# Performance work log

Hardware: AMD Instinct MI355X
Metric: run time of the kernel (lower is better)

## Reference

```python
import math
import jax, jax.numpy as jnp
import numpy as np

H = 16  # head_count
D = 1024  # model_dim
DH = D // H  # dim_per_head = 64
PAD_IDX = 1


def setup_inputs() -> dict:
    key = jax.random.key(0)
    ks = jax.random.split(key, 16)
    B, L = 4, 512
    s = 0.02
    inp = {
        'key': jax.random.normal(ks[0], (B, L, D), jnp.float32),
        'value': jax.random.normal(ks[1], (B, L, D), jnp.float32),
        'query': jax.random.normal(ks[2], (B, L, D), jnp.float32),
        'ast_parents_matrix': jax.random.randint(ks[3], (B, L, L), 0, 200, jnp.int32),
        'mask': jnp.zeros((B, 1, L), jnp.bool_),
        'Wq': jax.random.normal(ks[4], (D, D), jnp.float32) * s,
        'bq': jnp.zeros((D,), jnp.float32),
        'Wk': jax.random.normal(ks[5], (D, D), jnp.float32) * s,
        'bk': jnp.zeros((D,), jnp.float32),
        'Wv': jax.random.normal(ks[6], (D, D), jnp.float32) * s,
        'bv': jnp.zeros((D,), jnp.float32),
        'Wo': jax.random.normal(ks[7], (D, D), jnp.float32) * s,
        'bo': jnp.zeros((D,), jnp.float32),
        'struct_emb': jax.random.normal(ks[8], (200, DH), jnp.float32).at[PAD_IDX].set(0.0),
        'value_emb': jax.random.normal(ks[9], (10000, DH), jnp.float32).at[PAD_IDX].set(0.0),
    }
    return inp


def _parent_embeddings(matrix, struct_emb, value_emb):
    # matrix: (B, Lq, K) int ids; even key positions use structure vocab, odd use value vocab
    B, Lq, K = matrix.shape
    s_ids = matrix[:, :, ::2]   # (B, Lq, ceil(K/2))
    v_ids = matrix[:, :, 1::2]  # (B, Lq, floor(K/2))
    emb_s = struct_emb[s_ids]   # (B, Lq, S, DH)
    emb_v = value_emb[v_ids]    # (B, Lq, V, DH)
    S = emb_s.shape[2]
    if emb_v.shape[2] != S:  # odd K: pad value stream by one zero slot, drop after interleave
        emb_v = jnp.concatenate([emb_v, jnp.zeros_like(emb_s[:, :, :1])], axis=2)
    pe = jnp.stack([emb_s, emb_v], axis=3).reshape(B, Lq, 2 * S, DH)
    return pe[:, :, :K, :]  # (B, Lq, K, DH)


def reference(key, value, query, ast_parents_matrix, mask,
              Wq, bq, Wk, bk, Wv, bv, Wo, bo, struct_emb, value_emb):
    B, L, _ = query.shape

    def shape(x):
        return x.reshape(B, -1, H, DH).transpose(0, 2, 1, 3)  # (B,H,L,DH)

    q = shape(query @ Wq + bq) / math.sqrt(DH)
    k = shape(key @ Wk + bk)
    v = shape(value @ Wv + bv)

    qk = jnp.einsum('bhid,bhjd->bhij', q, k)  # (B,H,L,L)

    pe = _parent_embeddings(ast_parents_matrix[:, :, :L], struct_emb, value_emb)
    score_ast = jnp.einsum('bhid,bijd->bhij', q, pe)

    scores = (qk + score_ast).astype(jnp.float32)
    scores = jnp.where(mask[:, None, :, :], -1e18, scores)  # mask: (B,1,L)->(B,1,1,L)
    attn = jax.nn.softmax(scores, axis=-1).astype(q.dtype)
    # dropout p=0.0 (eval) -> identity
    context = jnp.einsum('bhij,bhjd->bhid', attn, v)  # (B,H,L,DH)
    context = context.transpose(0, 2, 1, 3).reshape(B, L, D)
    output = context @ Wo + bo
    return output, attn
```

## Files before the change

### kernel.cpp

```cpp
#include <hip/hip_runtime.h>
#include <cstddef>

#define H 16
#define D 1024
#define DH 64
#define L 512

typedef __attribute__((ext_vector_type(8))) short bf16x8;
typedef __attribute__((ext_vector_type(4))) short bf16x4;
typedef __attribute__((ext_vector_type(4))) float f32x4;

__device__ inline short f2bf(float x) {
    union { float f; unsigned u; } c; c.f = x;
    unsigned r = (c.u + 0x7FFFu + ((c.u >> 16) & 1u)) >> 16;
    return (short)r;
}
__device__ inline float bf2f(short x) {
    union { float f; unsigned u; } c;
    c.u = ((unsigned)(unsigned short)x) << 16; return c.f;
}

struct CvtArgs { const float* src[5]; short* dst[5]; int n[5]; };

__global__ __launch_bounds__(256) void cvt_kernel(CvtArgs a) {
    int r = blockIdx.y;
    const float* s = a.src[r];
    short* d = a.dst[r];
    int n = a.n[r];
    int i = (blockIdx.x * 256 + threadIdx.x) * 8;
    if (i >= n) return;
    float4 x0 = *(const float4*)(s + i);
    float4 x1 = *(const float4*)(s + i + 4);
    bf16x8 o;
    o[0] = f2bf(x0.x); o[1] = f2bf(x0.y); o[2] = f2bf(x0.z); o[3] = f2bf(x0.w);
    o[4] = f2bf(x1.x); o[5] = f2bf(x1.y); o[6] = f2bf(x1.z); o[7] = f2bf(x1.w);
    *(bf16x8*)(d + i) = o;
}

struct WtArgs { const float* W[4]; short* T[4]; };

__global__ __launch_bounds__(256) void wtrans_kernel(WtArgs a) {
    const float* W = a.W[blockIdx.z];
    short* T = a.T[blockIdx.z];
    int idx = blockIdx.x * 256 + threadIdx.x;
    int n = idx & 1023;
    int k0 = (idx >> 10) << 3;
    bf16x8 o;
    #pragma unroll
    for (int kk = 0; kk < 8; ++kk)
        o[kk] = f2bf(W[(size_t)(k0 + kk) * 1024 + n]);
    *(bf16x8*)(T + (size_t)n * 1024 + k0) = o;
}

#define BM 128
#define BN 64
#define BKK 64

__global__ __launch_bounds__(256) void gemm_bf16_kernel(
    const short* __restrict__ A, const short* __restrict__ Bt,
    const float* __restrict__ bias, void* __restrict__ out,
    int M, int N, int K, float scale, int mode)
{
    __shared__ short As[BM][BKK + 8];
    __shared__ short Bs[BN][BKK + 8];
    const int tid = threadIdx.x;
    const int m0 = blockIdx.y * BM;
    const int n0 = blockIdx.x * BN;
    const int wave = tid >> 6, lane = tid & 63;
    const int fm = lane & 15, quad = lane >> 4;

    const int ar = tid >> 1, ah = (tid & 1) * 32;
    const int br = tid >> 2, bq = (tid & 3) * 16;

    f32x4 acc[2][4];
    #pragma unroll
    for (int mt = 0; mt < 2; ++mt)
        #pragma unroll
        for (int nt = 0; nt < 4; ++nt) acc[mt][nt] = (f32x4){0.f, 0.f, 0.f, 0.f};

    const short* Ag = A + (size_t)(m0 + ar) * K + ah;
    const short* Bg = Bt + (size_t)(n0 + br) * K + bq;

    for (int k0 = 0; k0 < K; k0 += BKK) {
        bf16x8 a0 = *(const bf16x8*)(Ag + k0);
        bf16x8 a1 = *(const bf16x8*)(Ag + k0 + 8);
        bf16x8 a2 = *(const bf16x8*)(Ag + k0 + 16);
        bf16x8 a3 = *(const bf16x8*)(Ag + k0 + 24);
        bf16x8 b0 = *(const bf16x8*)(Bg + k0);
        bf16x8 b1 = *(const bf16x8*)(Bg + k0 + 8);
        __syncthreads();
        *(bf16x8*)(&As[ar][ah])      = a0;
        *(bf16x8*)(&As[ar][ah + 8])  = a1;
        *(bf16x8*)(&As[ar][ah + 16]) = a2;
        *(bf16x8*)(&As[ar][ah + 24]) = a3;
        *(bf16x8*)(&Bs[br][bq])      = b0;
        *(bf16x8*)(&Bs[br][bq + 8])  = b1;
        __syncthreads();
        #pragma unroll
        for (int ks = 0; ks < BKK; ks += 32) {
            bf16x8 af[2], bfr[4];
            af[0] = *(const bf16x8*)(&As[wave * 32 + fm][ks + quad * 8]);
            af[1] = *(const bf16x8*)(&As[wave * 32 + 16 + fm][ks + quad * 8]);
            #pragma unroll
            for (int nt = 0; nt < 4; ++nt)
                bfr[nt] = *(const bf16x8*)(&Bs[nt * 16 + fm][ks + quad * 8]);
            #pragma unroll
            for (int mt = 0; mt < 2; ++mt)
                #pragma unroll
                for (int nt = 0; nt < 4; ++nt)
                    acc[mt][nt] = __builtin_amdgcn_mfma_f32_16x16x32_bf16(
                        af[mt], bfr[nt], acc[mt][nt], 0, 0, 0);
        }
    }

    if (mode == 2) {
        __syncthreads();
        short (*T)[BM + 8] = (short(*)[BM + 8])&As[0][0];
        #pragma unroll
        for (int mt = 0; mt < 2; ++mt)
            #pragma unroll
            for (int nt = 0; nt < 4; ++nt) {
                int nn = nt * 16 + fm;
                float bv = bias[n0 + nn];
                #pragma unroll
                for (int r = 0; r < 4; ++r) {
                    int mm = wave * 32 + mt * 16 + quad * 4 + r;
                    T[nn][mm] = f2bf((acc[mt][nt][r] + bv) * scale);
                }
            }
        __syncthreads();
        int b = m0 >> 9;
        int ibase = m0 & (L - 1);
        int hblk = n0 >> 6;
        int n = tid >> 2, seg = (tid & 3) * 32;
        short* dst = (short*)out + (((size_t)(b * H + hblk) * DH + n) * L) + ibase + seg;
        #pragma unroll
        for (int c = 0; c < 4; ++c)
            *(bf16x8*)(dst + c * 8) = *(const bf16x8*)(&T[n][seg + c * 8]);
    } else {
        #pragma unroll
        for (int mt = 0; mt < 2; ++mt)
            #pragma unroll
            for (int nt = 0; nt < 4; ++nt) {
                int n = n0 + nt * 16 + fm;
                float bv = bias[n];
                #pragma unroll
                for (int r = 0; r < 4; ++r) {
                    int m = m0 + wave * 32 + mt * 16 + quad * 4 + r;
                    float val = (acc[mt][nt][r] + bv) * scale;
                    if (mode == 0) {
                        ((float*)out)[(size_t)m * N + n] = val;
                    } else {
                        int b = m >> 9, i = m & (L - 1);
                        int h = n >> 6, d = n & (DH - 1);
                        ((short*)out)[(((size_t)(b * H + h) * L + i) * DH) + d] = f2bf(val);
                    }
                }
            }
    }
}

__global__ __launch_bounds__(256) void ast_kernel(
    const short* __restrict__ Qb, const int* __restrict__ mat,
    const short* __restrict__ semb, const short* __restrict__ vemb,
    short* __restrict__ Sast)
{
    const int i = blockIdx.x, b = blockIdx.y;
    const int tid = threadIdx.x;
    const int wave = tid >> 6, lane = tid & 63;
    const int fm = lane & 15, quad = lane >> 4;
    __shared__ short Sl[H][L + 8];

    const short* qp = Qb + (((size_t)(b * H + fm) * L + i) * DH);
    bf16x8 a0 = *(const bf16x8*)(qp + quad * 8);
    bf16x8 a1 = *(const bf16x8*)(qp + 32 + quad * 8);

    const int* mrow = mat + ((size_t)b * L + i) * L;

    for (int jt = wave; jt < L / 16; jt += 4) {
        int j = jt * 16 + fm;
        int idx = mrow[j];
        const short* er = ((j & 1) ? vemb : semb) + (size_t)idx * DH;
        bf16x8 b0 = *(const bf16x8*)(er + quad * 8);
        bf16x8 b1 = *(const bf16x8*)(er + 32 + quad * 8);
        f32x4 c = {0.f, 0.f, 0.f, 0.f};
        c = __builtin_amdgcn_mfma_f32_16x16x32_bf16(a0, b0, c, 0, 0, 0);
        c = __builtin_amdgcn_mfma_f32_16x16x32_bf16(a1, b1, c, 0, 0, 0);
        #pragma unroll
        for (int r = 0; r < 4; ++r)
            Sl[quad * 4 + r][j] = f2bf(c[r]);
    }
    __syncthreads();
    int hh = tid >> 4, j0 = (tid & 15) * 32;
    short* dst = Sast + ((((size_t)b * L + i) * H + hh) * L) + j0;
    #pragma unroll
    for (int c = 0; c < 4; ++c)
        *(bf16x8*)(dst + c * 8) = *(const bf16x8*)(&Sl[hh][j0 + c * 8]);
}

__global__ __launch_bounds__(256) void attn_fused_kernel(
    const short* __restrict__ Qb, const short* __restrict__ Kb,
    const short* __restrict__ Vt, const short* __restrict__ Sast,
    const unsigned char* __restrict__ mask,
    float* __restrict__ attn, short* __restrict__ ctx)
{
    const int i0 = blockIdx.x * 16;
    const int h = blockIdx.y;
    const int b = blockIdx.z;
    const int tid = threadIdx.x;
    const int wave = tid >> 6, lane = tid & 63;
    const int fm = lane & 15, quad = lane >> 4;

    __shared__ float S[16][L + 4];
    __shared__ short Pb[16][L + 8];

    {
        int r = tid >> 4, c0 = (tid & 15) * 32;
        const short* sp = Sast + ((((size_t)b * L + i0 + r) * H + h) * L) + c0;
        #pragma unroll
        for (int c = 0; c < 4; ++c)
            *(bf16x8*)(&Pb[r][c0 + c * 8]) = *(const bf16x8*)(sp + c * 8);
    }
    __syncthreads();

    const short* qp = Qb + (((size_t)(b * H + h) * L + i0 + fm) * DH);
    bf16x8 a0 = *(const bf16x8*)(qp + quad * 8);
    bf16x8 a1 = *(const bf16x8*)(qp + 32 + quad * 8);
    const short* Kbase = Kb + ((size_t)(b * H + h) * L) * DH;

    for (int jt = wave; jt < L / 16; jt += 4) {
        int j = jt * 16 + fm;
        const short* kr = Kbase + (size_t)j * DH;
        bf16x8 b0 = *(const bf16x8*)(kr + quad * 8);
        bf16x8 b1 = *(const bf16x8*)(kr + 32 + quad * 8);
        f32x4 c = {0.f, 0.f, 0.f, 0.f};
        c = __builtin_amdgcn_mfma_f32_16x16x32_bf16(a0, b0, c, 0, 0, 0);
        c = __builtin_amdgcn_mfma_f32_16x16x32_bf16(a1, b1, c, 0, 0, 0);
        bool mk = mask[(size_t)b * L + j] != 0;
        #pragma unroll
        for (int r = 0; r < 4; ++r) {
            int ir = quad * 4 + r;
            S[ir][j] = mk ? -1e18f : (c[r] + bf2f(Pb[ir][j]));
        }
    }
    __syncthreads();

    #pragma unroll
    for (int rr = 0; rr < 4; ++rr) {
        int r = wave * 4 + rr;
        float mx = -3.0e38f;
        #pragma unroll
        for (int it = 0; it < 2; ++it) {
            float4 v = *(const float4*)(&S[r][lane * 4 + it * 256]);
            mx = fmaxf(mx, fmaxf(fmaxf(v.x, v.y), fmaxf(v.z, v.w)));
        }
        #pragma unroll
        for (int off = 32; off > 0; off >>= 1) mx = fmaxf(mx, __shfl_xor(mx, off));
        float sum = 0.f;
        #pragma unroll
        for (int it = 0; it < 2; ++it) {
            float4 v = *(const float4*)(&S[r][lane * 4 + it * 256]);
            v.x = __expf(v.x - mx); v.y = __expf(v.y - mx);
            v.z = __expf(v.z - mx); v.w = __expf(v.w - mx);
            *(float4*)(&S[r][lane * 4 + it * 256]) = v;
            sum += v.x + v.y + v.z + v.w;
        }
        #pragma unroll
        for (int off = 32; off > 0; off >>= 1) sum += __shfl_xor(sum, off);
        float inv = 1.f / sum;
        float* arow = attn + (((size_t)(b * H + h) * L + i0 + r) * L);
        #pragma unroll
        for (int it = 0; it < 2; ++it) {
            int j4 = lane * 4 + it * 256;
            float4 v = *(const float4*)(&S[r][j4]);
            v.x *= inv; v.y *= inv; v.z *= inv; v.w *= inv;
            *(float4*)(arow + j4) = v;
            bf16x4 pk;
            pk[0] = f2bf(v.x); pk[1] = f2bf(v.y); pk[2] = f2bf(v.z); pk[3] = f2bf(v.w);
            *(bf16x4*)(&Pb[r][j4]) = pk;
        }
    }
    __syncthreads();

    const short* Vb = Vt + (((size_t)(b * H + h) * DH + wave * 16 + fm) * L);
    f32x4 o = {0.f, 0.f, 0.f, 0.f};
    for (int ks = 0; ks < L; ks += 32) {
        bf16x8 pa = *(const bf16x8*)(&Pb[fm][ks + quad * 8]);
        bf16x8 vb = *(const bf16x8*)(Vb + ks + quad * 8);
        o = __builtin_amdgcn_mfma_f32_16x16x32_bf16(pa, vb, o, 0, 0, 0);
    }
    #pragma unroll
    for (int r = 0; r < 4; ++r)
        ctx[((size_t)b * L + i0 + quad * 4 + r) * D + h * DH + wave * 16 + fm] = f2bf(o[r]);
}

extern "C" void kernel_launch(void* const* d_in, const int* in_sizes, int n_in,
                              void* d_out, int out_size, void* d_ws, size_t ws_size,
                              hipStream_t stream) {
    const float* key_in   = (const float*)d_in[0];
    const float* value_in = (const float*)d_in[1];
    const float* query_in = (const float*)d_in[2];
    const int*   mat      = (const int*)d_in[3];
    const unsigned char* mask = (const unsigned char*)d_in[4];
    const float* Wq = (const float*)d_in[5];
    const float* bq = (const float*)d_in[6];
    const float* Wk = (const float*)d_in[7];
    const float* bk = (const float*)d_in[8];
    const float* Wv = (const float*)d_in[9];
    const float* bv = (const float*)d_in[10];
    const float* Wo = (const float*)d_in[11];
    const float* bo = (const float*)d_in[12];
    const float* struct_emb = (const float*)d_in[13];
    const float* value_emb  = (const float*)d_in[14];

    const int B = in_sizes[2] / (L * D);
    const int M = B * L;

    short* p = (short*)d_ws;
    short* xk  = p;  p += (size_t)M * D;
    short* xv  = p;  p += (size_t)M * D;
    short* xq  = p;  p += (size_t)M * D;
    short* WqT = p;  p += (size_t)D * D;
    short* WkT = p;  p += (size_t)D * D;
    short* WvT = p;  p += (size_t)D * D;
    short* WoT = p;  p += (size_t)D * D;
    short* semb = p; p += 16384;
    short* vemb = p; p += (size_t)in_sizes[14];
    short* Qb = p;   p += (size_t)M * D;
    short* Kb = p;   p += (size_t)M * D;
    short* Vt = p;   p += (size_t)M * D;
    short* Sast = p; p += (size_t)B * L * H * L;
    short* ctx = xk;

    float* out_p  = (float*)d_out;
    float* attn_p = out_p + (size_t)M * D;

    CvtArgs ca;
    ca.src[0] = key_in;     ca.dst[0] = xk;   ca.n[0] = M * D;
    ca.src[1] = value_in;   ca.dst[1] = xv;   ca.n[1] = M * D;
    ca.src[2] = query_in;   ca.dst[2] = xq;   ca.n[2] = M * D;
    ca.src[3] = struct_emb; ca.dst[3] = semb; ca.n[3] = in_sizes[13];
    ca.src[4] = value_emb;  ca.dst[4] = vemb; ca.n[4] = in_sizes[14];
    cvt_kernel<<<dim3((M * D) / 2048, 5), 256, 0, stream>>>(ca);

    WtArgs wa;
    wa.W[0] = Wq; wa.W[1] = Wk; wa.W[2] = Wv; wa.W[3] = Wo;
    wa.T[0] = WqT; wa.T[1] = WkT; wa.T[2] = WvT; wa.T[3] = WoT;
    wtrans_kernel<<<dim3(512, 1, 4), 256, 0, stream>>>(wa);

    dim3 gg(D / BN, M / BM);
    gemm_bf16_kernel<<<gg, 256, 0, stream>>>(xq, WqT, bq, Qb, M, D, D, 0.125f, 1);
    gemm_bf16_kernel<<<gg, 256, 0, stream>>>(xk, WkT, bk, Kb, M, D, D, 1.0f, 1);
    gemm_bf16_kernel<<<gg, 256, 0, stream>>>(xv, WvT, bv, Vt, M, D, D, 1.0f, 2);

    ast_kernel<<<dim3(L, B), 256, 0, stream>>>(Qb, mat, semb, vemb, Sast);

    attn_fused_kernel<<<dim3(L / 16, H, B), 256, 0, stream>>>(
        Qb, Kb, Vt, Sast, mask, attn_p, ctx);

    gemm_bf16_kernel<<<gg, 256, 0, stream>>>(ctx, WoT, bo, out_p, M, D, D, 1.0f, 0);
}
```

Before: 294.0 us.

## Use direct global-to-LDS loads with swizzle, batch QKV GEMMs, register-resident softmax

The GEMM now stages tiles with global_load_lds (direct DMA into LDS) using an XOR-swizzled layout to avoid bank conflicts, and the Q/K/V projections are merged into one launch via a z-indexed batch. The attention kernel keeps scores in registers, does the row max and sum with shuffles plus a small cross-wave LDS reduction, and drops the large float score buffer and the Sast preload into LDS. This cuts LDS traffic, launch count and shared memory use, which may raise occupancy. The trade-offs are more register pressure and uncoalesced per-element attn stores.

```diff
diff --git a/kernel.cpp b/kernel.cpp
--- a/kernel.cpp
+++ b/kernel.cpp
@@ -18,6 +18,13 @@
 __device__ inline float bf2f(short x) {
     union { float f; unsigned u; } c;
     c.u = ((unsigned)(unsigned short)x) << 16; return c.f;
+}
+
+__device__ inline void gload_lds16(const void* g, void* l) {
+    __builtin_amdgcn_global_load_lds(
+        (const __attribute__((address_space(1))) unsigned int*)g,
+        (__attribute__((address_space(3))) unsigned int*)l,
+        16, 0, 0);
 }
 
 struct CvtArgs { const float* src[5]; short* dst[5]; int n[5]; };
@@ -56,21 +63,62 @@
 #define BN 64
 #define BKK 64
 
-__global__ __launch_bounds__(256) void gemm_bf16_kernel(
-    const short* __restrict__ A, const short* __restrict__ Bt,
-    const float* __restrict__ bias, void* __restrict__ out,
-    int M, int N, int K, float scale, int mode)
-{
-    __shared__ short As[BM][BKK + 8];
-    __shared__ short Bs[BN][BKK + 8];
+struct GemmBatch {
+    const short* A[3]; const short* Bt[3]; const float* bias[3];
+    void* out[3]; float scale[3]; int mode[3];
+};
+
+__global__ __launch_bounds__(256) void gemm_mfma_kernel(GemmBatch P, int M, int N, int K) {
+    const int z = blockIdx.z;
+    const short* __restrict__ A  = P.A[z];
+    const short* __restrict__ Bt = P.Bt[z];
+    const float* __restrict__ bias = P.bias[z];
+    const float scale = P.scale[z];
+    const int mode = P.mode[z];
+
+    __shared__ short lds[(BM + BN) * BKK];
+    short* As = lds;
+    short* Bs = lds + BM * BKK;
+
     const int tid = threadIdx.x;
-    const int m0 = blockIdx.y * BM;
-    const int n0 = blockIdx.x * BN;
     const int wave = tid >> 6, lane = tid & 63;
     const int fm = lane & 15, quad = lane >> 4;
-
-    const int ar = tid >> 1, ah = (tid & 1) * 32;
-    const int br = tid >> 2, bq = (tid & 3) * 16;
+    const int m0 = blockIdx.y * BM, n0 = blockIdx.x * BN;
+
+    int arow[4], acol[4];
+    #pragma unroll
+    for (int t = 0; t < 4; ++t) {
+        int s = (wave * 4 + t) * 64 + lane;
+        int row = s >> 3;
+        int u = (s & 7) ^ (row & 7);
+        arow[t] = row; acol[t] = u * 8;
+    }
+    int brow[2], bcol[2];
+    #pragma unroll
+    for (int t = 0; t < 2; ++t) {
+        int s = (wave * 2 + t) * 64 + lane;
+        int row = s >> 3;
+        int u = (s & 7) ^ (row & 7);
+        brow[t] = row; bcol[t] = u * 8;
+    }
+
+    int aoff[2][2], boff[4][2];
+    #pragma unroll
+    for (int mt = 0; mt < 2; ++mt)
+        #pragma unroll
+        for (int kst = 0; kst < 2; ++kst) {
+            int row = wave * 32 + mt * 16 + fm;
+            int u = quad + 4 * kst;
+            aoff[mt][kst] = row * 64 + ((u ^ (row & 7)) * 8);
+        }
+    #pragma unroll
+    for (int nt = 0; nt < 4; ++nt)
+        #pragma unroll
+        for (int kst = 0; kst < 2; ++kst) {
+            int row = nt * 16 + fm;
+            int u = quad + 4 * kst;
+            boff[nt][kst] = row * 64 + ((u ^ (row & 7)) * 8);
+        }
 
     f32x4 acc[2][4];
     #pragma unroll
@@ -78,32 +126,25 @@
         #pragma unroll
         for (int nt = 0; nt < 4; ++nt) acc[mt][nt] = (f32x4){0.f, 0.f, 0.f, 0.f};
 
-    const short* Ag = A + (size_t)(m0 + ar) * K + ah;
-    const short* Bg = Bt + (size_t)(n0 + br) * K + bq;
-
     for (int k0 = 0; k0 < K; k0 += BKK) {
-        bf16x8 a0 = *(const bf16x8*)(Ag + k0);
-        bf16x8 a1 = *(const bf16x8*)(Ag + k0 + 8);
-        bf16x8 a2 = *(const bf16x8*)(Ag + k0 + 16);
-        bf16x8 a3 = *(const bf16x8*)(Ag + k0 + 24);
-        bf16x8 b0 = *(const bf16x8*)(Bg + k0);
-        bf16x8 b1 = *(const bf16x8*)(Bg + k0 + 8);
         __syncthreads();
-        *(bf16x8*)(&As[ar][ah])      = a0;
-        *(bf16x8*)(&As[ar][ah + 8])  = a1;
-        *(bf16x8*)(&As[ar][ah + 16]) = a2;
-        *(bf16x8*)(&As[ar][ah + 24]) = a3;
-        *(bf16x8*)(&Bs[br][bq])      = b0;
-        *(bf16x8*)(&Bs[br][bq + 8])  = b1;
+        #pragma unroll
+        for (int t = 0; t < 4; ++t)
+            gload_lds16(A + (size_t)(m0 + arow[t]) * K + k0 + acol[t],
+                        As + (wave * 4 + t) * 512);
+        #pragma unroll
+        for (int t = 0; t < 2; ++t)
+            gload_lds16(Bt + (size_t)(n0 + brow[t]) * K + k0 + bcol[t],
+                        Bs + (wave * 2 + t) * 512);
         __syncthreads();
         #pragma unroll
-        for (int ks = 0; ks < BKK; ks += 32) {
+        for (int kst = 0; kst < 2; ++kst) {
             bf16x8 af[2], bfr[4];
-            af[0] = *(const bf16x8*)(&As[wave * 32 + fm][ks + quad * 8]);
-            af[1] = *(const bf16x8*)(&As[wave * 32 + 16 + fm][ks + quad * 8]);
+            af[0] = *(const bf16x8*)(As + aoff[0][kst]);
+            af[1] = *(const bf16x8*)(As + aoff[1][kst]);
             #pragma unroll
             for (int nt = 0; nt < 4; ++nt)
-                bfr[nt] = *(const bf16x8*)(&Bs[nt * 16 + fm][ks + quad * 8]);
+                bfr[nt] = *(const bf16x8*)(Bs + boff[nt][kst]);
             #pragma unroll
             for (int mt = 0; mt < 2; ++mt)
                 #pragma unroll
@@ -115,7 +156,7 @@
 
     if (mode == 2) {
         __syncthreads();
-        short (*T)[BM + 8] = (short(*)[BM + 8])&As[0][0];
+        short (*T)[BM + 8] = (short(*)[BM + 8])&lds[0];
         #pragma unroll
         for (int mt = 0; mt < 2; ++mt)
             #pragma unroll
@@ -133,7 +174,7 @@
         int ibase = m0 & (L - 1);
         int hblk = n0 >> 6;
         int n = tid >> 2, seg = (tid & 3) * 32;
-        short* dst = (short*)out + (((size_t)(b * H + hblk) * DH + n) * L) + ibase + seg;
+        short* dst = (short*)P.out[z] + (((size_t)(b * H + hblk) * DH + n) * L) + ibase + seg;
         #pragma unroll
         for (int c = 0; c < 4; ++c)
             *(bf16x8*)(dst + c * 8) = *(const bf16x8*)(&T[n][seg + c * 8]);
@@ -149,11 +190,11 @@
                     int m = m0 + wave * 32 + mt * 16 + quad * 4 + r;
                     float val = (acc[mt][nt][r] + bv) * scale;
                     if (mode == 0) {
-                        ((float*)out)[(size_t)m * N + n] = val;
+                        ((float*)P.out[z])[(size_t)m * N + n] = val;
                     } else {
                         int b = m >> 9, i = m & (L - 1);
                         int h = n >> 6, d = n & (DH - 1);
-                        ((short*)out)[(((size_t)(b * H + h) * L + i) * DH) + d] = f2bf(val);
+                        ((short*)P.out[z])[(((size_t)(b * H + h) * L + i) * DH) + d] = f2bf(val);
                     }
                 }
             }
@@ -211,24 +252,22 @@
     const int wave = tid >> 6, lane = tid & 63;
     const int fm = lane & 15, quad = lane >> 4;
 
-    __shared__ float S[16][L + 4];
     __shared__ short Pb[16][L + 8];
-
-    {
-        int r = tid >> 4, c0 = (tid & 15) * 32;
-        const short* sp = Sast + ((((size_t)b * L + i0 + r) * H + h) * L) + c0;
-        #pragma unroll
-        for (int c = 0; c < 4; ++c)
-            *(bf16x8*)(&Pb[r][c0 + c * 8]) = *(const bf16x8*)(sp + c * 8);
-    }
-    __syncthreads();
+    __shared__ float red_m[4][16];
+    __shared__ float red_l[4][16];
 
     const short* qp = Qb + (((size_t)(b * H + h) * L + i0 + fm) * DH);
     bf16x8 a0 = *(const bf16x8*)(qp + quad * 8);
     bf16x8 a1 = *(const bf16x8*)(qp + 32 + quad * 8);
     const short* Kbase = Kb + ((size_t)(b * H + h) * L) * DH;
-
-    for (int jt = wave; jt < L / 16; jt += 4) {
+    const short* Sb = Sast + (((size_t)b * L + i0) * H + h) * L;
+
+    float s[8][4];
+    float mx[4] = {-3.0e38f, -3.0e38f, -3.0e38f, -3.0e38f};
+
+    #pragma unroll
+    for (int t = 0; t < 8; ++t) {
+        int jt = wave + t * 4;
         int j = jt * 16 + fm;
         const short* kr = Kbase + (size_t)j * DH;
         bf16x8 b0 = *(const bf16x8*)(kr + quad * 8);
@@ -240,44 +279,64 @@
         #pragma unroll
         for (int r = 0; r < 4; ++r) {
             int ir = quad * 4 + r;
-            S[ir][j] = mk ? -1e18f : (c[r] + bf2f(Pb[ir][j]));
-        }
-    }
+            float sv = c[r] + bf2f(Sb[(size_t)ir * H * L + j]);
+            sv = mk ? -1e18f : sv;
+            s[t][r] = sv;
+            mx[r] = fmaxf(mx[r], sv);
+        }
+    }
+
+    #pragma unroll
+    for (int off = 1; off <= 8; off <<= 1)
+        #pragma unroll
+        for (int r = 0; r < 4; ++r)
+            mx[r] = fmaxf(mx[r], __shfl_xor(mx[r], off));
+    if (fm == 0)
+        #pragma unroll
+        for (int r = 0; r < 4; ++r) red_m[wave][quad * 4 + r] = mx[r];
     __syncthreads();
-
-    #pragma unroll
-    for (int rr = 0; rr < 4; ++rr) {
-        int r = wave * 4 + rr;
-        float mx = -3.0e38f;
-        #pragma unroll
-        for (int it = 0; it < 2; ++it) {
-            float4 v = *(const float4*)(&S[r][lane * 4 + it * 256]);
-            mx = fmaxf(mx, fmaxf(fmaxf(v.x, v.y), fmaxf(v.z, v.w)));
-        }
-        #pragma unroll
-        for (int off = 32; off > 0; off >>= 1) mx = fmaxf(mx, __shfl_xor(mx, off));
-        float sum = 0.f;
-        #pragma unroll
-        for (int it = 0; it < 2; ++it) {
-            float4 v = *(const float4*)(&S[r][lane * 4 + it * 256]);
-            v.x = __expf(v.x - mx); v.y = __expf(v.y - mx);
-            v.z = __expf(v.z - mx); v.w = __expf(v.w - mx);
-            *(float4*)(&S[r][lane * 4 + it * 256]) = v;
-            sum += v.x + v.y + v.z + v.w;
-        }
-        #pragma unroll
-        for (int off = 32; off > 0; off >>= 1) sum += __shfl_xor(sum, off);
-        float inv = 1.f / sum;
-        float* arow = attn + (((size_t)(b * H + h) * L + i0 + r) * L);
-        #pragma unroll
-        for (int it = 0; it < 2; ++it) {
-            int j4 = lane * 4 + it * 256;
-            float4 v = *(const float4*)(&S[r][j4]);
-            v.x *= inv; v.y *= inv; v.z *= inv; v.w *= inv;
-            *(float4*)(arow + j4) = v;
-            bf16x4 pk;
-            pk[0] = f2bf(v.x); pk[1] = f2bf(v.y); pk[2] = f2bf(v.z); pk[3] = f2bf(v.w);
-            *(bf16x4*)(&Pb[r][j4]) = pk;
+    float M_[4];
+    #pragma unroll
+    for (int r = 0; r < 4; ++r) {
+        int ir = quad * 4 + r;
+        M_[r] = fmaxf(fmaxf(red_m[0][ir], red_m[1][ir]),
+                      fmaxf(red_m[2][ir], red_m[3][ir]));
+    }
+
+    float sum[4] = {0.f, 0.f, 0.f, 0.f};
+    #pragma unroll
+    for (int t = 0; t < 8; ++t)
+        #pragma unroll
+        for (int r = 0; r < 4; ++r) {
+            float e = __expf(s[t][r] - M_[r]);
+            s[t][r] = e;
+            sum[r] += e;
+        }
+    #pragma unroll
+    for (int off = 1; off <= 8; off <<= 1)
+        #pragma unroll
+        for (int r = 0; r < 4; ++r)
+            sum[r] += __shfl_xor(sum[r], off);
+    if (fm == 0)
+        #pragma unroll
+        for (int r = 0; r < 4; ++r) red_l[wave][quad * 4 + r] = sum[r];
+    __syncthreads();
+    float inv[4];
+    #pragma unroll
+    for (int r = 0; r < 4; ++r) {
+        int ir = quad * 4 + r;
+        inv[r] = 1.f / (red_l[0][ir] + red_l[1][ir] + red_l[2][ir] + red_l[3][ir]);
+    }
+
+    #pragma unroll
+    for (int t = 0; t < 8; ++t) {
+        int j = (wave + t * 4) * 16 + fm;
+        #pragma unroll
+        for (int r = 0; r < 4; ++r) {
+            int ir = quad * 4 + r;
+            float p = s[t][r] * inv[r];
+            attn[(((size_t)(b * H + h) * L + i0 + ir) * L) + j] = p;
+            Pb[ir][j] = f2bf(p);
         }
     }
     __syncthreads();
@@ -348,15 +407,20 @@
     wa.T[0] = WqT; wa.T[1] = WkT; wa.T[2] = WvT; wa.T[3] = WoT;
     wtrans_kernel<<<dim3(512, 1, 4), 256, 0, stream>>>(wa);
 
-    dim3 gg(D / BN, M / BM);
-    gemm_bf16_kernel<<<gg, 256, 0, stream>>>(xq, WqT, bq, Qb, M, D, D, 0.125f, 1);
-    gemm_bf16_kernel<<<gg, 256, 0, stream>>>(xk, WkT, bk, Kb, M, D, D, 1.0f, 1);
-    gemm_bf16_kernel<<<gg, 256, 0, stream>>>(xv, WvT, bv, Vt, M, D, D, 1.0f, 2);
+    GemmBatch qkv;
+    qkv.A[0] = xq; qkv.Bt[0] = WqT; qkv.bias[0] = bq; qkv.out[0] = Qb; qkv.scale[0] = 0.125f; qkv.mode[0] = 1;
+    qkv.A[1] = xk; qkv.Bt[1] = WkT; qkv.bias[1] = bk; qkv.out[1] = Kb; qkv.scale[1] = 1.0f;   qkv.mode[1] = 1;
+    qkv.A[2] = xv; qkv.Bt[2] = WvT; qkv.bias[2] = bv; qkv.out[2] = Vt; qkv.scale[2] = 1.0f;   qkv.mode[2] = 2;
+    gemm_mfma_kernel<<<dim3(D / BN, M / BM, 3), 256, 0, stream>>>(qkv, M, D, D);
 
     ast_kernel<<<dim3(L, B), 256, 0, stream>>>(Qb, mat, semb, vemb, Sast);
 
     attn_fused_kernel<<<dim3(L / 16, H, B), 256, 0, stream>>>(
         Qb, Kb, Vt, Sast, mask, attn_p, ctx);
 
-    gemm_bf16_kernel<<<gg, 256, 0, stream>>>(ctx, WoT, bo, out_p, M, D, D, 1.0f, 0);
-}
+    GemmBatch fin;
+    fin.A[0] = ctx; fin.Bt[0] = WoT; fin.bias[0] = bo; fin.out[0] = out_p; fin.scale[0] = 1.0f; fin.mode[0] = 0;
+    fin.A[1] = ctx; fin.Bt[1] = WoT; fin.bias[1] = bo; fin.out[1] = out_p; fin.scale[1] = 1.0f; fin.mode[1] = 0;
+    fin.A[2] = ctx; fin.Bt[2] = WoT; fin.bias[2] = bo; fin.out[2] = out_p; fin.scale[2] = 1.0f; fin.mode[2] = 0;
+    gemm_mfma_kernel<<<dim3(D / BN, M / BM, 1), 256, 0, stream>>>(fin, M, D, D);
+}
```

Measured after the change: 242.0 us. 1.21x faster.
